# Performance work log

Measured on AMD Instinct MI355X. Metric: run time of the kernel, lower is better.

The kernel has to match this reference:

```python
import jax, jax.numpy as jnp
import numpy as np

B, N, M = 4, 8192, 1024
IN_DIM, OUT_DIM = 512, 256


def setup_inputs() -> dict:
    key = jax.random.key(0)
    k1, k2, k3 = jax.random.split(key, 3)
    features = jax.random.normal(k1, (B, N, OUT_DIM), dtype=jnp.float32)
    prompt = jax.random.normal(k2, (B, M, IN_DIM), dtype=jnp.float32)
    # torch nn.Linear weight layout: [out_dim, in_dim]; y = x @ W^T
    W = jax.random.normal(k3, (OUT_DIM, IN_DIM), dtype=jnp.float32) * (1.0 / np.sqrt(IN_DIM))
    return {"features": features, "prompt": prompt, "W": W}


def reference(features, prompt, W):
    # prompt_proj (no bias): [B, M, in_dim] -> [B, M, out_dim]
    reduced = jnp.einsum('bmi,oi->bmo', prompt, W)
    # unscaled single-head cross-attention (original computes emb_dim but never divides by it)
    scores = jnp.einsum('bnd,bmd->bnm', features, reduced)  # [B, N, M]
    attn = jax.nn.softmax(scores, axis=-1)
    attn_val = jnp.einsum('bnm,bmd->bnd', attn, reduced)    # [B, N, out_dim]
    return features + attn_val  # residual (tgt = src.clone())
```

## Files before the change

### kernel.cpp

```cpp
#include <hip/hip_runtime.h>

typedef _Float16 f16;
typedef __bf16   bf16;
typedef _Float16 f16x4  __attribute__((ext_vector_type(4)));
typedef _Float16 f16x8  __attribute__((ext_vector_type(8)));
typedef __bf16   bf16x2 __attribute__((ext_vector_type(2)));
typedef __bf16   bf16x8 __attribute__((ext_vector_type(8)));
typedef float    f32x4  __attribute__((ext_vector_type(4)));
typedef float    f32x16 __attribute__((ext_vector_type(16)));
typedef unsigned int u32;

#define B_   4
#define N_   8192
#define M_   1024
#define IND_ 512
#define D_   256
#define CFIX 60.0f

__device__ __forceinline__ void gload_lds16(const void* g, void* l) {
    __builtin_amdgcn_global_load_lds(
        (const __attribute__((address_space(1))) u32*)g,
        (__attribute__((address_space(3))) u32*)l, 16, 0, 0);
}

__global__ __launch_bounds__(256) void k_proj(const float* __restrict__ prompt,
                                              const float* __restrict__ W,
                                              f16* __restrict__ red,
                                              bf16* __restrict__ redT)
{
    __shared__ __align__(16) f16 Wt[2][128 * 72];

    const int tid  = threadIdx.x;
    const int w    = tid >> 6;
    const int lane = tid & 63;
    const int nl = lane & 15, qq = lane >> 4;
    const int mtile = blockIdx.x >> 1, chalf = blockIdx.x & 1;
    const int m0 = mtile * 16, c0 = chalf * 128;

    f32x4 acc[2];
#pragma unroll
    for (int i = 0; i < 2; ++i)
#pragma unroll
        for (int r = 0; r < 4; ++r) acc[i][r] = 0.f;

    f32x4 wr[8];
#define LOADW(KT)                                                           \
    {                                                                       \
        _Pragma("unroll")                                                   \
        for (int j = 0; j < 8; ++j) {                                       \
            const int c = tid + 256 * j;                                    \
            wr[j] = *(const f32x4*)(W + (size_t)(c0 + (c >> 4)) * IND_      \
                                    + (KT) + (c & 15) * 4);                 \
        }                                                                   \
    }

    LOADW(0);
    for (int it = 0; it < 8; ++it) {
        const int bi = it & 1;
#pragma unroll
        for (int j = 0; j < 8; ++j) {
            const int c = tid + 256 * j;
            f16x4 h;
#pragma unroll
            for (int e = 0; e < 4; ++e) h[e] = (f16)wr[j][e];
            *(f16x4*)&Wt[bi][(c >> 4) * 72 + (c & 15) * 4] = h;
        }
        __syncthreads();
        if (it < 7) LOADW((it + 1) * 64);

        const int kt = it * 64;
        const float* ap = prompt + (size_t)(m0 + nl) * IND_ + kt + qq * 8;
        f32x4 a[2][2];
        a[0][0] = *(const f32x4*)ap;        a[0][1] = *(const f32x4*)(ap + 4);
        a[1][0] = *(const f32x4*)(ap + 32); a[1][1] = *(const f32x4*)(ap + 36);
#pragma unroll
        for (int kc = 0; kc < 2; ++kc) {
            f16x8 ahi, alo;
#pragma unroll
            for (int e = 0; e < 4; ++e) {
                ahi[e]     = (f16)a[kc][0][e];  alo[e]     = (f16)(a[kc][0][e] - (float)ahi[e]);
                ahi[4 + e] = (f16)a[kc][1][e];  alo[4 + e] = (f16)(a[kc][1][e] - (float)ahi[4 + e]);
            }
#pragma unroll
            for (int dbi = 0; dbi < 2; ++dbi) {
                f16x8 bw = *(const f16x8*)&Wt[bi][(w * 32 + dbi * 16 + nl) * 72
                                                  + kc * 32 + qq * 8];
                acc[dbi] = __builtin_amdgcn_mfma_f32_16x16x32_f16(ahi, bw, acc[dbi], 0, 0, 0);
                acc[dbi] = __builtin_amdgcn_mfma_f32_16x16x32_f16(alo, bw, acc[dbi], 0, 0, 0);
            }
        }
        __syncthreads();
    }

#pragma unroll
    for (int dbi = 0; dbi < 2; ++dbi) {
        const int col = c0 + w * 32 + dbi * 16 + nl;
#pragma unroll
        for (int r = 0; r < 4; ++r) {
            const int row = m0 + qq * 4 + r;
            const float v = acc[dbi][r];
            red[(size_t)row * D_ + col] = (f16)v;
            const int bb = row >> 10, mm = row & 1023;
            redT[(((size_t)bb * 32 + (mm >> 5)) * D_ + col) * 32 + (mm & 31)] = (bf16)v;
        }
    }
}

__global__ __launch_bounds__(256, 2) void k_attn(const float* __restrict__ feat,
                                                 const f16* __restrict__ red,
                                                 const bf16* __restrict__ redT,
                                                 float* __restrict__ out)
{
    __shared__ __align__(16) f16  Kb[2][32 * 256];
    __shared__ __align__(16) bf16 Vb[2][256 * 32];

    const int tid  = threadIdx.x;
    const int wid  = tid >> 6;
    const int lane = tid & 63;
    const int nl2  = lane & 31;
    const int half = lane >> 5;
    const int qg   = wid >> 1;
    const int h2   = wid & 1;

    const int bid = blockIdx.x;
    const int xcd = bid & 7, i64 = bid >> 3;
    const int b   = xcd >> 1;
    const int jj  = (xcd & 1) * 64 + i64;
    const int qrow = jj * 64 + qg * 32;

    const char* kbase = (const char*)(red  + (size_t)b * M_ * D_);
    const char* vbase = (const char*)(redT + (size_t)b * 32 * D_ * 32);

    f16x8 qf[16];
#pragma unroll
    for (int kc = 0; kc < 16; ++kc) {
        const float* fp = feat + ((size_t)b * N_ + qrow + nl2) * D_ + kc * 16 + half * 8;
        f32x4 f0 = *(const f32x4*)fp;
        f32x4 f1 = *(const f32x4*)(fp + 4);
        f16x8 v;
#pragma unroll
        for (int e = 0; e < 4; ++e) { v[e] = (f16)f0[e]; v[4 + e] = (f16)f1[e]; }
        qf[kc] = v;
    }

    f32x16 O[4];
#pragma unroll
    for (int nb = 0; nb < 4; ++nb)
#pragma unroll
        for (int r = 0; r < 16; ++r) O[nb][r] = 0.f;
    f32x16 Ol;
#pragma unroll
    for (int r = 0; r < 16; ++r) Ol[r] = 0.f;

    bf16x8 ones;
#pragma unroll
    for (int e = 0; e < 8; ++e) ones[e] = (bf16)1.0f;

    const int vsw = (nl2 >> 1) & 3;

#define STG(KT, BI)                                                           \
    {                                                                         \
        _Pragma("unroll")                                                     \
        for (int j = 0; j < 4; ++j) {                                         \
            const int c  = j * 256 + tid;                                     \
            const int kr = c >> 5;                                            \
            const int kj = (c & 31) ^ kr;                                     \
            gload_lds16(kbase + (size_t)((KT) + kr) * 512 + kj * 16,          \
                        &Kb[BI][(j * 256 + wid * 64) * 8]);                   \
            const int vd = c >> 2;                                            \
            const int vj = (c & 3) ^ ((vd >> 1) & 3);                         \
            gload_lds16(vbase + (size_t)((KT) >> 5) * 16384 + (size_t)vd * 64 + vj * 16, \
                        &Vb[BI][(j * 256 + wid * 64) * 8]);                   \
        }                                                                     \
    }

    STG(0, 0);
    for (int it = 0; it < 32; ++it) {
        __syncthreads();
        if (it < 31) STG((it + 1) * 32, (it + 1) & 1);
        const int bi = it & 1;

        f32x16 s0, s1;
#pragma unroll
        for (int r = 0; r < 16; ++r) { s0[r] = 0.f; s1[r] = 0.f; }
        __builtin_amdgcn_s_setprio(1);
#pragma unroll
        for (int kc = 0; kc < 8; ++kc) {
            f16x8 kb0 = *(const f16x8*)&Kb[bi][nl2 * 256 + ((((2 * kc)     * 2 + half) ^ nl2) * 8)];
            f16x8 kb1 = *(const f16x8*)&Kb[bi][nl2 * 256 + ((((2 * kc + 1) * 2 + half) ^ nl2) * 8)];
            s0 = __builtin_amdgcn_mfma_f32_32x32x16_f16(kb0, qf[2 * kc],     s0, 0, 0, 0);
            s1 = __builtin_amdgcn_mfma_f32_32x32x16_f16(kb1, qf[2 * kc + 1], s1, 0, 0, 0);
        }
        __builtin_amdgcn_s_setprio(0);

        float p[16];
#pragma unroll
        for (int r = 0; r < 16; ++r) p[r] = __expf(s0[r] + s1[r] - CFIX);
        u32 w[8];
#pragma unroll
        for (int i = 0; i < 8; ++i) {
            union { bf16x2 h; u32 u; } t;
            t.h = (bf16x2){ (bf16)p[2 * i], (bf16)p[2 * i + 1] };
            w[i] = t.u;
        }
        const u32 sa = half ? w[0] : w[2], sb = half ? w[1] : w[3];
        const u32 sc = half ? w[4] : w[6], sd = half ? w[5] : w[7];
        const u32 ra = (u32)__shfl_xor((int)sa, 32);
        const u32 rb = (u32)__shfl_xor((int)sb, 32);
        const u32 rc = (u32)__shfl_xor((int)sc, 32);
        const u32 rd = (u32)__shfl_xor((int)sd, 32);
        union { u32 u[4]; bf16x8 h; } U0, U1;
        U0.u[0] = half ? ra : w[0];  U0.u[1] = half ? rb : w[1];
        U0.u[2] = half ? w[2] : ra;  U0.u[3] = half ? w[3] : rb;
        U1.u[0] = half ? rc : w[4];  U1.u[1] = half ? rd : w[5];
        U1.u[2] = half ? w[6] : rc;  U1.u[3] = half ? w[7] : rd;
        const bf16x8 pa0 = U0.h, pa1 = U1.h;

        __builtin_amdgcn_s_setprio(1);
        Ol = __builtin_amdgcn_mfma_f32_32x32x16_bf16(pa0, ones, Ol, 0, 0, 0);
        Ol = __builtin_amdgcn_mfma_f32_32x32x16_bf16(pa1, ones, Ol, 0, 0, 0);
#pragma unroll
        for (int nb = 0; nb < 4; ++nb) {
            const int n0 = h2 * 128 + nb * 32 + nl2;
            bf16x8 v0 = *(const bf16x8*)&Vb[bi][n0 * 32 + ((half ^ vsw) * 8)];
            O[nb] = __builtin_amdgcn_mfma_f32_32x32x16_bf16(pa0, v0, O[nb], 0, 0, 0);
            bf16x8 v1 = *(const bf16x8*)&Vb[bi][n0 * 32 + (((2 + half) ^ vsw) * 8)];
            O[nb] = __builtin_amdgcn_mfma_f32_32x32x16_bf16(pa1, v1, O[nb], 0, 0, 0);
        }
        __builtin_amdgcn_s_setprio(0);
    }

    float inv[16];
#pragma unroll
    for (int r = 0; r < 16; ++r) inv[r] = 1.0f / Ol[r];
#pragma unroll
    for (int nb = 0; nb < 4; ++nb)
#pragma unroll
        for (int r = 0; r < 16; ++r) {
            const int row = (r & 3) + 8 * (r >> 2) + 4 * half;
            const size_t idx = ((size_t)b * N_ + qrow + row) * D_ + h2 * 128 + nb * 32 + nl2;
            out[idx] = feat[idx] + O[nb][r] * inv[r];
        }
}

extern "C" void kernel_launch(void* const* d_in, const int* in_sizes, int n_in,
                              void* d_out, int out_size, void* d_ws, size_t ws_size,
                              hipStream_t stream)
{
    const float* feat   = (const float*)d_in[0];
    const float* prompt = (const float*)d_in[1];
    const float* W      = (const float*)d_in[2];
    float* out = (float*)d_out;

    f16*  red  = (f16*)d_ws;
    bf16* redT = (bf16*)((char*)d_ws + (size_t)2 * 1024 * 1024);

    k_proj<<<dim3(512), 256, 0, stream>>>(prompt, W, red, redT);
    k_attn<<<dim3(512), 256, 0, stream>>>(feat, red, redT, out);
}
```

Before: 164.1 us.

## Fuse projection and attention kernels with a software grid barrier

Merges the prompt projection and attention kernels into one persistent launch of 512 blocks. A global atomic counter barrier separates the two phases, and the query-fragment load is placed before the barrier so it overlaps with the wait. This removes one kernel launch and the gap between kernels. It depends on all 512 blocks being co-resident (2 per CU on 256 CUs) or it deadlocks, and it adds atomic spin overhead.

After: 290.8 us. 1.77x slower.

```diff
diff --git a/kernel.cpp b/kernel.cpp
--- a/kernel.cpp
+++ b/kernel.cpp
@@ -17,119 +17,113 @@
 #define D_   256
 #define CFIX 60.0f
 
+__device__ unsigned g_bar = 0;
+
 __device__ __forceinline__ void gload_lds16(const void* g, void* l) {
     __builtin_amdgcn_global_load_lds(
         (const __attribute__((address_space(1))) u32*)g,
         (__attribute__((address_space(3))) u32*)l, 16, 0, 0);
 }
 
-__global__ __launch_bounds__(256) void k_proj(const float* __restrict__ prompt,
-                                              const float* __restrict__ W,
-                                              f16* __restrict__ red,
-                                              bf16* __restrict__ redT)
+__global__ __launch_bounds__(256, 2) void k_fused(const float* __restrict__ feat,
+                                                  const float* __restrict__ prompt,
+                                                  const float* __restrict__ W,
+                                                  f16* __restrict__ red,
+                                                  bf16* __restrict__ redT,
+                                                  float* __restrict__ out)
 {
-    __shared__ __align__(16) f16 Wt[2][128 * 72];
-
-    const int tid  = threadIdx.x;
-    const int w    = tid >> 6;
-    const int lane = tid & 63;
-    const int nl = lane & 15, qq = lane >> 4;
-    const int mtile = blockIdx.x >> 1, chalf = blockIdx.x & 1;
-    const int m0 = mtile * 16, c0 = chalf * 128;
-
-    f32x4 acc[2];
-#pragma unroll
-    for (int i = 0; i < 2; ++i)
-#pragma unroll
-        for (int r = 0; r < 4; ++r) acc[i][r] = 0.f;
-
-    f32x4 wr[8];
-#define LOADW(KT)                                                           \
-    {                                                                       \
-        _Pragma("unroll")                                                   \
-        for (int j = 0; j < 8; ++j) {                                       \
-            const int c = tid + 256 * j;                                    \
-            wr[j] = *(const f32x4*)(W + (size_t)(c0 + (c >> 4)) * IND_      \
-                                    + (KT) + (c & 15) * 4);                 \
-        }                                                                   \
-    }
-
-    LOADW(0);
-    for (int it = 0; it < 8; ++it) {
-        const int bi = it & 1;
-#pragma unroll
-        for (int j = 0; j < 8; ++j) {
-            const int c = tid + 256 * j;
-            f16x4 h;
-#pragma unroll
-            for (int e = 0; e < 4; ++e) h[e] = (f16)wr[j][e];
-            *(f16x4*)&Wt[bi][(c >> 4) * 72 + (c & 15) * 4] = h;
-        }
-        __syncthreads();
-        if (it < 7) LOADW((it + 1) * 64);
-
-        const int kt = it * 64;
-        const float* ap = prompt + (size_t)(m0 + nl) * IND_ + kt + qq * 8;
-        f32x4 a[2][2];
-        a[0][0] = *(const f32x4*)ap;        a[0][1] = *(const f32x4*)(ap + 4);
-        a[1][0] = *(const f32x4*)(ap + 32); a[1][1] = *(const f32x4*)(ap + 36);
-#pragma unroll
-        for (int kc = 0; kc < 2; ++kc) {
-            f16x8 ahi, alo;
-#pragma unroll
-            for (int e = 0; e < 4; ++e) {
-                ahi[e]     = (f16)a[kc][0][e];  alo[e]     = (f16)(a[kc][0][e] - (float)ahi[e]);
-                ahi[4 + e] = (f16)a[kc][1][e];  alo[4 + e] = (f16)(a[kc][1][e] - (float)ahi[4 + e]);
-            }
-#pragma unroll
-            for (int dbi = 0; dbi < 2; ++dbi) {
-                f16x8 bw = *(const f16x8*)&Wt[bi][(w * 32 + dbi * 16 + nl) * 72
-                                                  + kc * 32 + qq * 8];
-                acc[dbi] = __builtin_amdgcn_mfma_f32_16x16x32_f16(ahi, bw, acc[dbi], 0, 0, 0);
-                acc[dbi] = __builtin_amdgcn_mfma_f32_16x16x32_f16(alo, bw, acc[dbi], 0, 0, 0);
-            }
-        }
-        __syncthreads();
-    }
-
-#pragma unroll
-    for (int dbi = 0; dbi < 2; ++dbi) {
-        const int col = c0 + w * 32 + dbi * 16 + nl;
-#pragma unroll
-        for (int r = 0; r < 4; ++r) {
-            const int row = m0 + qq * 4 + r;
-            const float v = acc[dbi][r];
-            red[(size_t)row * D_ + col] = (f16)v;
-            const int bb = row >> 10, mm = row & 1023;
-            redT[(((size_t)bb * 32 + (mm >> 5)) * D_ + col) * 32 + (mm & 31)] = (bf16)v;
-        }
-    }
-}
-
-__global__ __launch_bounds__(256, 2) void k_attn(const float* __restrict__ feat,
-                                                 const f16* __restrict__ red,
-                                                 const bf16* __restrict__ redT,
-                                                 float* __restrict__ out)
-{
-    __shared__ __align__(16) f16  Kb[2][32 * 256];
-    __shared__ __align__(16) bf16 Vb[2][256 * 32];
+    __shared__ __align__(16) char smem[65536];
 
     const int tid  = threadIdx.x;
     const int wid  = tid >> 6;
     const int lane = tid & 63;
+    const int bid  = blockIdx.x;
+
+    {
+        f16* Wt = (f16*)smem;
+        const int nl = lane & 15, qq = lane >> 4;
+        const int mtile = bid >> 1, chalf = bid & 1;
+        const int m0 = mtile * 16, c0 = chalf * 128;
+
+        f32x4 acc[2];
+#pragma unroll
+        for (int i = 0; i < 2; ++i)
+#pragma unroll
+            for (int r = 0; r < 4; ++r) acc[i][r] = 0.f;
+
+        f32x4 wr[8];
+#define LOADW(KT)                                                           \
+        {                                                                   \
+            _Pragma("unroll")                                               \
+            for (int j = 0; j < 8; ++j) {                                   \
+                const int c = tid + 256 * j;                                \
+                wr[j] = *(const f32x4*)(W + (size_t)(c0 + (c >> 4)) * IND_  \
+                                        + (KT) + (c & 15) * 4);             \
+            }                                                               \
+        }
+
+        LOADW(0);
+        for (int it = 0; it < 8; ++it) {
+            const int bi = it & 1;
+#pragma unroll
+            for (int j = 0; j < 8; ++j) {
+                const int c = tid + 256 * j;
+                f16x4 h;
+#pragma unroll
+                for (int e = 0; e < 4; ++e) h[e] = (f16)wr[j][e];
+                *(f16x4*)&Wt[bi * (128 * 72) + (c >> 4) * 72 + (c & 15) * 4] = h;
+            }
+            __syncthreads();
+            if (it < 7) LOADW((it + 1) * 64);
+
+            const int kt = it * 64;
+            const float* ap = prompt + (size_t)(m0 + nl) * IND_ + kt + qq * 8;
+            f32x4 a[2][2];
+            a[0][0] = *(const f32x4*)ap;        a[0][1] = *(const f32x4*)(ap + 4);
+            a[1][0] = *(const f32x4*)(ap + 32); a[1][1] = *(const f32x4*)(ap + 36);
+#pragma unroll
+            for (int kc = 0; kc < 2; ++kc) {
+                f16x8 ahi, alo;
+#pragma unroll
+                for (int e = 0; e < 4; ++e) {
+                    ahi[e]     = (f16)a[kc][0][e];  alo[e]     = (f16)(a[kc][0][e] - (float)ahi[e]);
+                    ahi[4 + e] = (f16)a[kc][1][e];  alo[4 + e] = (f16)(a[kc][1][e] - (float)ahi[4 + e]);
+                }
+#pragma unroll
+                for (int dbi = 0; dbi < 2; ++dbi) {
+                    f16x8 bw = *(const f16x8*)&Wt[bi * (128 * 72)
+                                                  + (wid * 32 + dbi * 16 + nl) * 72
+                                                  + kc * 32 + qq * 8];
+                    acc[dbi] = __builtin_amdgcn_mfma_f32_16x16x32_f16(ahi, bw, acc[dbi], 0, 0, 0);
+                    acc[dbi] = __builtin_amdgcn_mfma_f32_16x16x32_f16(alo, bw, acc[dbi], 0, 0, 0);
+                }
+            }
+            __syncthreads();
+        }
+#undef LOADW
+
+#pragma unroll
+        for (int dbi = 0; dbi < 2; ++dbi) {
+            const int col = c0 + wid * 32 + dbi * 16 + nl;
+#pragma unroll
+            for (int r = 0; r < 4; ++r) {
+                const int row = m0 + qq * 4 + r;
+                const float v = acc[dbi][r];
+                red[(size_t)row * D_ + col] = (f16)v;
+                const int bb = row >> 10, mm = row & 1023;
+                redT[(((size_t)bb * 32 + (mm >> 5)) * D_ + col) * 32 + (mm & 31)] = (bf16)v;
+            }
+        }
+    }
+
     const int nl2  = lane & 31;
     const int half = lane >> 5;
     const int qg   = wid >> 1;
     const int h2   = wid & 1;
-
-    const int bid = blockIdx.x;
     const int xcd = bid & 7, i64 = bid >> 3;
     const int b   = xcd >> 1;
     const int jj  = (xcd & 1) * 64 + i64;
     const int qrow = jj * 64 + qg * 32;
-
-    const char* kbase = (const char*)(red  + (size_t)b * M_ * D_);
-    const char* vbase = (const char*)(redT + (size_t)b * 32 * D_ * 32);
 
     f16x8 qf[16];
 #pragma unroll
@@ -142,6 +136,24 @@
         for (int e = 0; e < 4; ++e) { v[e] = (f16)f0[e]; v[4 + e] = (f16)f1[e]; }
         qf[kc] = v;
     }
+
+    __threadfence();
+    __syncthreads();
+    if (tid == 0) {
+        const unsigned old    = atomicAdd(&g_bar, 1u);
+        const unsigned target = old - (old % 512u) + 512u;
+        while (__hip_atomic_load(&g_bar, __ATOMIC_ACQUIRE,
+                                 __HIP_MEMORY_SCOPE_AGENT) < target)
+            __builtin_amdgcn_s_sleep(32);
+    }
+    __syncthreads();
+    __threadfence();
+
+    f16*  Kb = (f16*)smem;
+    bf16* Vb = (bf16*)(smem + 32768);
+
+    const char* kbase = (const char*)(red  + (size_t)b * M_ * D_);
+    const char* vbase = (const char*)(redT + (size_t)b * 32 * D_ * 32);
 
     f32x16 O[4];
 #pragma unroll
@@ -166,11 +178,11 @@
             const int kr = c >> 5;                                            \
             const int kj = (c & 31) ^ kr;                                     \
             gload_lds16(kbase + (size_t)((KT) + kr) * 512 + kj * 16,          \
-                        &Kb[BI][(j * 256 + wid * 64) * 8]);                   \
+                        &Kb[(BI) * 8192 + (j * 256 + wid * 64) * 8]);         \
             const int vd = c >> 2;                                            \
             const int vj = (c & 3) ^ ((vd >> 1) & 3);                         \
             gload_lds16(vbase + (size_t)((KT) >> 5) * 16384 + (size_t)vd * 64 + vj * 16, \
-                        &Vb[BI][(j * 256 + wid * 64) * 8]);                   \
+                        &Vb[(BI) * 8192 + (j * 256 + wid * 64) * 8]);         \
         }                                                                     \
     }
 
@@ -186,8 +198,8 @@
         __builtin_amdgcn_s_setprio(1);
 #pragma unroll
         for (int kc = 0; kc < 8; ++kc) {
-            f16x8 kb0 = *(const f16x8*)&Kb[bi][nl2 * 256 + ((((2 * kc)     * 2 + half) ^ nl2) * 8)];
-            f16x8 kb1 = *(const f16x8*)&Kb[bi][nl2 * 256 + ((((2 * kc + 1) * 2 + half) ^ nl2) * 8)];
+            f16x8 kb0 = *(const f16x8*)&Kb[bi * 8192 + nl2 * 256 + ((((2 * kc)     * 2 + half) ^ nl2) * 8)];
+            f16x8 kb1 = *(const f16x8*)&Kb[bi * 8192 + nl2 * 256 + ((((2 * kc + 1) * 2 + half) ^ nl2) * 8)];
             s0 = __builtin_amdgcn_mfma_f32_32x32x16_f16(kb0, qf[2 * kc],     s0, 0, 0, 0);
             s1 = __builtin_amdgcn_mfma_f32_32x32x16_f16(kb1, qf[2 * kc + 1], s1, 0, 0, 0);
         }
@@ -222,13 +234,14 @@
 #pragma unroll
         for (int nb = 0; nb < 4; ++nb) {
             const int n0 = h2 * 128 + nb * 32 + nl2;
-            bf16x8 v0 = *(const bf16x8*)&Vb[bi][n0 * 32 + ((half ^ vsw) * 8)];
+            bf16x8 v0 = *(const bf16x8*)&Vb[bi * 8192 + n0 * 32 + ((half ^ vsw) * 8)];
             O[nb] = __builtin_amdgcn_mfma_f32_32x32x16_bf16(pa0, v0, O[nb], 0, 0, 0);
-            bf16x8 v1 = *(const bf16x8*)&Vb[bi][n0 * 32 + (((2 + half) ^ vsw) * 8)];
+            bf16x8 v1 = *(const bf16x8*)&Vb[bi * 8192 + n0 * 32 + (((2 + half) ^ vsw) * 8)];
             O[nb] = __builtin_amdgcn_mfma_f32_32x32x16_bf16(pa1, v1, O[nb], 0, 0, 0);
         }
         __builtin_amdgcn_s_setprio(0);
     }
+#undef STG
 
     float inv[16];
 #pragma unroll
@@ -255,6 +268,5 @@
     f16*  red  = (f16*)d_ws;
     bf16* redT = (bf16*)((char*)d_ws + (size_t)2 * 1024 * 1024);
 
-    k_proj<<<dim3(512), 256, 0, stream>>>(prompt, W, red, redT);
-    k_attn<<<dim3(512), 256, 0, stream>>>(feat, red, redT, out);
+    k_fused<<<dim3(512), 256, 0, stream>>>(feat, prompt, W, red, redT, out);
 }
```
